# Kernel tuning notes

Hardware: AMD Instinct MI355X
Metric: run time of the kernel (lower is better)

## Reference

```python
import jax, jax.numpy as jnp
import numpy as np

E_PHI = 1024
E_F = 1024
HID = 1024
N_HEADS = 16
HEAD_DIM = HID // N_HEADS


def setup_inputs() -> dict:
    key = jax.random.key(0)
    ks = jax.random.split(key, 9)
    B, S = 2, 2048
    s = 0.02
    return {
        "q": jax.random.normal(ks[0], (B, S, E_PHI), jnp.float32),
        "k": jax.random.normal(ks[1], (B, S, E_PHI), jnp.float32),
        "v": jax.random.normal(ks[2], (B, S, E_F), jnp.float32),
        "W_q": jax.random.normal(ks[3], (E_PHI, HID), jnp.float32) * s,
        "W_k": jax.random.normal(ks[4], (E_PHI, HID), jnp.float32) * s,
        "W_v": jax.random.normal(ks[5], (E_F, HID), jnp.float32) * s,
        "b_v": jax.random.normal(ks[6], (HID,), jnp.float32) * s,
        "W_o": jax.random.normal(ks[7], (HID, E_F), jnp.float32) * s,
        "b_o": jax.random.normal(ks[8], (E_F,), jnp.float32) * s,
    }


def reference(q, k, v, W_q, W_k, W_v, b_v, W_o, b_o):
    B, S, _ = q.shape
    # projections -> [B, S, n_heads, head_dim]
    qh = (q @ W_q).reshape(B, S, N_HEADS, HEAD_DIM)
    kh = (k @ W_k).reshape(B, S, N_HEADS, HEAD_DIM)
    vh = (v @ W_v + b_v).reshape(B, S, N_HEADS, HEAD_DIM)

    scale = 1.0 / jnp.sqrt(jnp.float32(HEAD_DIM))
    # scores: [B, H, S_q, S_k]
    scores = jnp.einsum("bihd,bjhd->bhij", qh, kh) * scale

    i = jnp.arange(S)[:, None]
    j = jnp.arange(S)[None, :]
    # strict causal (j < i) plus the single (0,0) entry
    keep = (j < i) | ((i == 0) & (j == 0))
    scores = jnp.where(keep, scores, jnp.float32(-jnp.inf))

    probs = jax.nn.softmax(scores, axis=-1)
    attn = jnp.einsum("bhij,bjhd->bihd", probs, vh).reshape(B, S, HID)
    # dropout is identity in eval mode
    return attn @ W_o + b_o
```

## Files before the change

### kernel.cpp

```cpp
#include <hip/hip_runtime.h>
#include <hip/hip_bf16.h>

typedef __attribute__((ext_vector_type(8))) short bf16x8;
typedef __attribute__((ext_vector_type(4))) float f32x4;
typedef __attribute__((ext_vector_type(4))) unsigned u32x4;

typedef __attribute__((address_space(1))) const void gv_t;
typedef __attribute__((address_space(3))) void lv_t;

static __device__ __forceinline__ void gload16(const void* g, void* l) {
    __builtin_amdgcn_global_load_lds((gv_t*)g, (lv_t*)l, 16, 0, 0);
}

static __device__ __forceinline__ f32x4 mfma16(bf16x8 a, bf16x8 b, f32x4 c) {
    return __builtin_amdgcn_mfma_f32_16x16x32_bf16(a, b, c, 0, 0, 0);
}

static __device__ __forceinline__ unsigned short f2bf(float x) {
    __bf16 b = (__bf16)x;
    return __builtin_bit_cast(unsigned short, b);
}
static __device__ __forceinline__ unsigned pk2(float lo, float hi) {
    return (unsigned)f2bf(lo) | ((unsigned)f2bf(hi) << 16);
}

#define NN 1024
#define KK 1024
#define BK 32
#define NKT (KK / BK)
#define AP 72
#define SOFF2 17.3123404907f

__global__ void cvt3_k(const float* __restrict__ q, const float* __restrict__ k,
                       const float* __restrict__ v, unsigned short* __restrict__ dst)
{
    const int z = blockIdx.y;
    const float* src = (z == 0) ? q : (z == 1) ? k : v;
    unsigned short* d = dst + (size_t)z * 4194304u;
    const size_t i = ((size_t)blockIdx.x * 256 + threadIdx.x) * 8;
    float4 a = *reinterpret_cast<const float4*>(&src[i]);
    float4 b = *reinterpret_cast<const float4*>(&src[i + 4]);
    bf16x8 o;
    o[0] = (short)f2bf(a.x); o[1] = (short)f2bf(a.y);
    o[2] = (short)f2bf(a.z); o[3] = (short)f2bf(a.w);
    o[4] = (short)f2bf(b.x); o[5] = (short)f2bf(b.y);
    o[6] = (short)f2bf(b.z); o[7] = (short)f2bf(b.w);
    *reinterpret_cast<bf16x8*>(&d[i]) = o;
}

__global__ void trcvt_k(const float* __restrict__ w0, const float* __restrict__ w1,
                        const float* __restrict__ w2, const float* __restrict__ w3,
                        unsigned short* __restrict__ dst)
{
    const int z = blockIdx.z;
    const float* W = (z == 0) ? w0 : (z == 1) ? w1 : (z == 2) ? w2 : w3;
    unsigned short* D = dst + (size_t)z * 1048576u;
    __shared__ float t[32][33];
    const int tx = threadIdx.x, ty = threadIdx.y;
    const int x  = blockIdx.x * 32 + tx;
    const int y0 = blockIdx.y * 32;
    for (int i = ty; i < 32; i += 8) t[i][tx] = W[(size_t)(y0 + i) * 1024 + x];
    __syncthreads();
    const int xo = y0 + tx;
    for (int i = ty; i < 32; i += 8)
        D[(size_t)(blockIdx.x * 32 + i) * 1024 + xo] = f2bf(t[tx][i]);
}

template<int MODE, int TM, int MINB>
__global__ __launch_bounds__(256, MINB)
void gemm2_k(const unsigned short* __restrict__ Abase,
             const unsigned short* __restrict__ Btbase,
             void* __restrict__ Cbase,
             unsigned short* __restrict__ C2,
             const float* __restrict__ bias)
{
    constexpr int ACH = TM / 64;
    constexpr int NJ  = (TM == 128) ? 4 : 2;
    __shared__ unsigned short As[3][ACH * 2048];
    __shared__ unsigned short Bs[3][4096];

    const int f   = blockIdx.x;
    const int xcd = f & 7;
    const int g   = f >> 3;
    int z, bx, by;
    if (MODE == 0) {
        z  = g >> 5;
        const int rr = g & 31;
        bx = xcd * 4 + (rr & 3);
        by = rr >> 2;
    } else {
        z  = 0;
        bx = xcd * 8 + (g & 7);
        by = g >> 3;
    }

    const unsigned short* A  = Abase  + (size_t)z * 4194304u;
    const unsigned short* Bt = Btbase + (size_t)z * 1048576u;

    const int tid = threadIdx.x;
    const int wid = tid >> 6, lane = tid & 63;
    const int lg = lane >> 4, lc = lane & 15;
    const int brow = bx * TM;
    const int bcol = by * 128;
    const int wr = (TM == 128) ? (wid >> 1) * 64 : 0;
    const int wc = (TM == 128) ? (wid & 1) * 64  : wid * 32;

    const int srow = tid >> 2;
    const int scol = (tid & 3) * 8;

    f32x4 acc[4][NJ];
#pragma unroll
    for (int i = 0; i < 4; ++i)
#pragma unroll
        for (int j = 0; j < NJ; ++j) acc[i][j] = (f32x4){0.f, 0.f, 0.f, 0.f};

    auto issue_tile = [&](int kt, int c) {
        const int k0 = kt * BK;
#pragma unroll
        for (int ch = 0; ch < ACH; ++ch)
            gload16(&A[(size_t)(brow + ch * 64 + srow) * KK + k0 + scol], &As[c][ch * 2048 + tid * 8]);
        gload16(&Bt[(size_t)(bcol + srow)      * KK + k0 + scol], &Bs[c][tid * 8]);
        gload16(&Bt[(size_t)(bcol + 64 + srow) * KK + k0 + scol], &Bs[c][2048 + tid * 8]);
    };
    auto compute_tile = [&](int c) {
        bf16x8 af[4], bfr[NJ];
#pragma unroll
        for (int i = 0; i < 4; ++i)
            af[i] = *reinterpret_cast<const bf16x8*>(&As[c][(wr + i * 16 + lc) * 32 + lg * 8]);
#pragma unroll
        for (int j = 0; j < NJ; ++j)
            bfr[j] = *reinterpret_cast<const bf16x8*>(&Bs[c][(wc + j * 16 + lc) * 32 + lg * 8]);
#pragma unroll
        for (int i = 0; i < 4; ++i)
#pragma unroll
            for (int j = 0; j < NJ; ++j)
                acc[i][j] = mfma16(af[i], bfr[j], acc[i][j]);
    };

    issue_tile(0, 0);
    issue_tile(1, 1);

    int c0 = 0, c1 = 1, c2 = 2;
    for (int kt = 0; kt < NKT - 1; ++kt) {
        if (TM == 128) asm volatile("s_waitcnt vmcnt(4)" ::: "memory");
        else           asm volatile("s_waitcnt vmcnt(3)" ::: "memory");
        __builtin_amdgcn_s_barrier();
        __builtin_amdgcn_sched_barrier(0);
        if (kt + 2 < NKT) issue_tile(kt + 2, c2);
        compute_tile(c0);
        const int t = c0; c0 = c1; c1 = c2; c2 = t;
    }
    asm volatile("s_waitcnt vmcnt(0)" ::: "memory");
    __builtin_amdgcn_s_barrier();
    __builtin_amdgcn_sched_barrier(0);
    compute_tile(c0);

    float scale = 1.0f;
    const float* bp = nullptr;
    if (MODE == 0) { if (z == 0) scale = 0.18033688f; if (z == 2) bp = bias; }
    else           { bp = bias; }

    if (MODE == 0 && z == 2) {
#pragma unroll
        for (int j = 0; j < NJ; ++j) {
            const int col = bcol + wc + j * 16 + lc;
            const int h = col >> 6, d = col & 63;
            const float bb = bp[col];
#pragma unroll
            for (int i = 0; i < 4; ++i) {
                const int row0 = brow + wr + i * 16 + lg * 4;
                const int b = row0 >> 11, s0 = row0 & 2047;
                const size_t o = ((size_t)((b * 16 + h) * 64 + d)) * 2048u + s0;
                uint2 st;
                st.x = pk2(acc[i][j][0] + bb, acc[i][j][1] + bb);
                st.y = pk2(acc[i][j][2] + bb, acc[i][j][3] + bb);
                *reinterpret_cast<uint2*>(&C2[o]) = st;
            }
        }
    } else {
#pragma unroll
        for (int j = 0; j < NJ; ++j) {
            const int col = bcol + wc + j * 16 + lc;
            const float bb = bp ? bp[col] : 0.0f;
#pragma unroll
            for (int i = 0; i < 4; ++i) {
                const int row0 = brow + wr + i * 16 + lg * 4;
#pragma unroll
                for (int r = 0; r < 4; ++r) {
                    const float val = acc[i][j][r] * scale + bb;
                    if (MODE == 0)
                        ((unsigned short*)Cbase)[(size_t)z * 4194304u + (size_t)(row0 + r) * NN + col] = f2bf(val);
                    else
                        ((float*)Cbase)[(size_t)(row0 + r) * NN + col] = val;
                }
            }
        }
    }
}

__global__ __launch_bounds__(256, 4)
void attn_k(const unsigned short* __restrict__ qh,
            const unsigned short* __restrict__ kh,
            const unsigned short* __restrict__ vt,
            unsigned short* __restrict__ out)
{
    __shared__ unsigned short Ks[2][64 * AP];
    __shared__ unsigned short Vs[2][64 * AP];

    const int id = blockIdx.x;
    const int u  = id >> 5;
    const int qt = (u < 16) ? u : 47 - u;
    const int bh = (id & 7) * 4 + ((id >> 3) & 3);
    const int b = bh >> 4, h = bh & 15;
    const int tid = threadIdx.x, wid = tid >> 6, lane = tid & 63;
    const int lg = lane >> 4, lc = lane & 15;
    const int q0w = qt * 64 + wid * 16;

    const size_t base = (size_t)b * 2048u * 1024u + (size_t)h * 64u;
    const unsigned short* Qb  = qh + base;
    const unsigned short* Kb  = kh + base;
    const unsigned short* Vtb = vt + (size_t)bh * 131072u;

    const int r0 = tid >> 3, kof = (tid & 7) * 8;
    const int kperm = ((r0 & 12) << 1) | ((r0 >> 2) & 4) | (r0 & 3);

    bf16x8 qf[2];
#pragma unroll
    for (int s = 0; s < 2; ++s)
        qf[s] = *reinterpret_cast<const bf16x8*>(&Qb[(size_t)(q0w + lc) * 1024 + s * 32 + lg * 8]);

    f32x4 accT[4];
#pragma unroll
    for (int d = 0; d < 4; ++d) accT[d] = (f32x4){0.f, 0.f, 0.f, 0.f};
    float lsum = 0.f;

    bf16x8 ka0 = *reinterpret_cast<const bf16x8*>(&Kb [(size_t)(kperm)      * 1024 + kof]);
    bf16x8 ka1 = *reinterpret_cast<const bf16x8*>(&Kb [(size_t)(32 + kperm) * 1024 + kof]);
    bf16x8 va0 = *reinterpret_cast<const bf16x8*>(&Vtb[(size_t)(r0)      * 2048 + kof]);
    bf16x8 va1 = *reinterpret_cast<const bf16x8*>(&Vtb[(size_t)(32 + r0) * 2048 + kof]);

    for (int kt = 0; kt <= qt; ++kt) {
        const int cur = kt & 1;
        const int k0 = kt * 64;

        *reinterpret_cast<bf16x8*>(&Ks[cur][(r0)      * AP + kof]) = ka0;
        *reinterpret_cast<bf16x8*>(&Ks[cur][(32 + r0) * AP + kof]) = ka1;
        *reinterpret_cast<bf16x8*>(&Vs[cur][(r0)      * AP + kof]) = va0;
        *reinterpret_cast<bf16x8*>(&Vs[cur][(32 + r0) * AP + kof]) = va1;
        asm volatile("s_waitcnt lgkmcnt(0)" ::: "memory");
        __builtin_amdgcn_s_barrier();
        __builtin_amdgcn_sched_barrier(0);

        if (kt < qt) {
            const int kn = k0 + 64;
            ka0 = *reinterpret_cast<const bf16x8*>(&Kb [(size_t)(kn + kperm)      * 1024 + kof]);
            ka1 = *reinterpret_cast<const bf16x8*>(&Kb [(size_t)(kn + 32 + kperm) * 1024 + kof]);
            va0 = *reinterpret_cast<const bf16x8*>(&Vtb[(size_t)(r0)      * 2048 + kn + kof]);
            va1 = *reinterpret_cast<const bf16x8*>(&Vtb[(size_t)(32 + r0) * 2048 + kn + kof]);
        }

        f32x4 sc[4];
#pragma unroll
        for (int g = 0; g < 4; ++g) sc[g] = (f32x4){0.f, 0.f, 0.f, 0.f};
        __builtin_amdgcn_s_setprio(1);
#pragma unroll
        for (int s = 0; s < 2; ++s)
#pragma unroll
            for (int g = 0; g < 4; ++g) {
                bf16x8 kf = *reinterpret_cast<const bf16x8*>(
                    &Ks[cur][(g * 16 + lc) * AP + s * 32 + lg * 8]);
                sc[g] = mfma16(kf, qf[s], sc[g]);
            }
        __builtin_amdgcn_s_setprio(0);

        if (kt == qt) {
            const int qi = q0w + lc;
#pragma unroll
            for (int g = 0; g < 4; ++g)
#pragma unroll
                for (int r = 0; r < 4; ++r) {
                    const int ki = k0 + ((g & 2) << 4) + 8 * lg + 4 * (g & 1) + r;
                    const bool keep = (ki < qi) || (qi == 0 && ki == 0);
                    if (!keep) sc[g][r] = -1e30f;
                }
        }

        float p[4][4];
#pragma unroll
        for (int g = 0; g < 4; ++g)
#pragma unroll
            for (int r = 0; r < 4; ++r) {
                p[g][r] = exp2f(sc[g][r] - SOFF2);
                lsum += p[g][r];
            }

#pragma unroll
        for (int s = 0; s < 2; ++s) {
            u32x4 fr;
            fr[0] = pk2(p[2 * s][0],     p[2 * s][1]);
            fr[1] = pk2(p[2 * s][2],     p[2 * s][3]);
            fr[2] = pk2(p[2 * s + 1][0], p[2 * s + 1][1]);
            fr[3] = pk2(p[2 * s + 1][2], p[2 * s + 1][3]);
            bf16x8 pb = __builtin_bit_cast(bf16x8, fr);
            __builtin_amdgcn_s_setprio(1);
#pragma unroll
            for (int di = 0; di < 4; ++di) {
                bf16x8 vf = *reinterpret_cast<const bf16x8*>(
                    &Vs[cur][(di * 16 + lc) * AP + s * 32 + lg * 8]);
                accT[di] = mfma16(vf, pb, accT[di]);
            }
            __builtin_amdgcn_s_setprio(0);
        }
    }

    lsum += __shfl_xor(lsum, 16);
    lsum += __shfl_xor(lsum, 32);
    const float inv = 1.0f / lsum;

    const size_t orow = (size_t)(b * 2048 + q0w + lc) * 1024 + (size_t)h * 64 + lg * 4;
#pragma unroll
    for (int di = 0; di < 4; ++di) {
        unsigned lo  = pk2(accT[di][0] * inv, accT[di][1] * inv);
        unsigned hi2 = pk2(accT[di][2] * inv, accT[di][3] * inv);
        uint2 st; st.x = lo; st.y = hi2;
        *reinterpret_cast<uint2*>(&out[orow + di * 16]) = st;
    }
}

extern "C" void kernel_launch(void* const* d_in, const int* in_sizes, int n_in,
                              void* d_out, int out_size, void* d_ws, size_t ws_size,
                              hipStream_t stream)
{
    const float* q   = (const float*)d_in[0];
    const float* k   = (const float*)d_in[1];
    const float* v   = (const float*)d_in[2];
    const float* W_q = (const float*)d_in[3];
    const float* W_k = (const float*)d_in[4];
    const float* W_v = (const float*)d_in[5];
    const float* b_v = (const float*)d_in[6];
    const float* W_o = (const float*)d_in[7];
    const float* b_o = (const float*)d_in[8];

    char* w = (char*)d_ws;
    unsigned short* qkvb = (unsigned short*)w;
    unsigned short* Wt   = (unsigned short*)(w + 25165824);
    unsigned short* ph   = (unsigned short*)(w + 33554432);
    unsigned short* attn = (unsigned short*)(w + 58720256);
    unsigned short* vt   = ph + 2 * 4194304;

    cvt3_k <<<dim3(2048, 3, 1), 256, 0, stream>>>(q, k, v, qkvb);
    trcvt_k<<<dim3(32, 32, 4), dim3(32, 8, 1), 0, stream>>>(W_q, W_k, W_v, W_o, Wt);
    gemm2_k<0, 128, 3><<<dim3(768, 1, 1), 256, 0, stream>>>(qkvb, Wt, ph, vt, b_v);
    attn_k <<<dim3(1024, 1, 1), 256, 0, stream>>>(ph, ph + 4194304, vt, attn);
    gemm2_k<1, 64, 2><<<dim3(512, 1, 1), 256, 0, stream>>>(attn, Wt + 3 * 1048576, d_out, nullptr, b_o);
}
```

Before: 112.4 us.

## Double query tile per attention block to reuse K/V tiles across 128 rows

The attention kernel now gives each block 128 query rows instead of 64. Each wave handles two 16-row fragments, so each K/V tile loaded into shared memory feeds twice as many MFMAs. The grid is halved and the launch bounds drop to 2 waves per SIMD to make room for the doubled accumulators. The causal pairing of query blocks is kept, and fragments whose diagonal tile has already passed are skipped. The costs are lower occupancy, fewer blocks to hide latency, and some imbalance between the two fragments of a wave.

```diff
diff --git a/kernel.cpp b/kernel.cpp
--- a/kernel.cpp
+++ b/kernel.cpp
@@ -198,7 +198,7 @@
     }
 }
 
-__global__ __launch_bounds__(256, 4)
+__global__ __launch_bounds__(256, 2)
 void attn_k(const unsigned short* __restrict__ qh,
             const unsigned short* __restrict__ kh,
             const unsigned short* __restrict__ vt,
@@ -209,12 +209,15 @@
 
     const int id = blockIdx.x;
     const int u  = id >> 5;
-    const int qt = (u < 16) ? u : 47 - u;
+    const int qb = (u < 8) ? u : 23 - u;
     const int bh = (id & 7) * 4 + ((id >> 3) & 3);
     const int b = bh >> 4, h = bh & 15;
     const int tid = threadIdx.x, wid = tid >> 6, lane = tid & 63;
     const int lg = lane >> 4, lc = lane & 15;
-    const int q0w = qt * 64 + wid * 16;
+    const int q0 = qb * 128 + wid * 32;
+    const int dt0 = q0 >> 6;
+    const int dt1 = (q0 + 16) >> 6;
+    const int nkt = 2 * qb + 2;
 
     const size_t base = (size_t)b * 2048u * 1024u + (size_t)h * 64u;
     const unsigned short* Qb  = qh + base;
@@ -224,22 +227,27 @@
     const int r0 = tid >> 3, kof = (tid & 7) * 8;
     const int kperm = ((r0 & 12) << 1) | ((r0 >> 2) & 4) | (r0 & 3);
 
-    bf16x8 qf[2];
-#pragma unroll
-    for (int s = 0; s < 2; ++s)
-        qf[s] = *reinterpret_cast<const bf16x8*>(&Qb[(size_t)(q0w + lc) * 1024 + s * 32 + lg * 8]);
-
-    f32x4 accT[4];
-#pragma unroll
-    for (int d = 0; d < 4; ++d) accT[d] = (f32x4){0.f, 0.f, 0.f, 0.f};
-    float lsum = 0.f;
+    bf16x8 qf[2][2];
+#pragma unroll
+    for (int f = 0; f < 2; ++f)
+#pragma unroll
+        for (int s = 0; s < 2; ++s)
+            qf[f][s] = *reinterpret_cast<const bf16x8*>(
+                &Qb[(size_t)(q0 + f * 16 + lc) * 1024 + s * 32 + lg * 8]);
+
+    f32x4 accT[2][4];
+#pragma unroll
+    for (int f = 0; f < 2; ++f)
+#pragma unroll
+        for (int d = 0; d < 4; ++d) accT[f][d] = (f32x4){0.f, 0.f, 0.f, 0.f};
+    float lsum[2] = {0.f, 0.f};
 
     bf16x8 ka0 = *reinterpret_cast<const bf16x8*>(&Kb [(size_t)(kperm)      * 1024 + kof]);
     bf16x8 ka1 = *reinterpret_cast<const bf16x8*>(&Kb [(size_t)(32 + kperm) * 1024 + kof]);
     bf16x8 va0 = *reinterpret_cast<const bf16x8*>(&Vtb[(size_t)(r0)      * 2048 + kof]);
     bf16x8 va1 = *reinterpret_cast<const bf16x8*>(&Vtb[(size_t)(32 + r0) * 2048 + kof]);
 
-    for (int kt = 0; kt <= qt; ++kt) {
+    for (int kt = 0; kt < nkt; ++kt) {
         const int cur = kt & 1;
         const int k0 = kt * 64;
 
@@ -251,7 +259,7 @@
         __builtin_amdgcn_s_barrier();
         __builtin_amdgcn_sched_barrier(0);
 
-        if (kt < qt) {
+        if (kt + 1 < nkt) {
             const int kn = k0 + 64;
             ka0 = *reinterpret_cast<const bf16x8*>(&Kb [(size_t)(kn + kperm)      * 1024 + kof]);
             ka1 = *reinterpret_cast<const bf16x8*>(&Kb [(size_t)(kn + 32 + kperm) * 1024 + kof]);
@@ -259,9 +267,15 @@
             va1 = *reinterpret_cast<const bf16x8*>(&Vtb[(size_t)(32 + r0) * 2048 + kn + kof]);
         }
 
-        f32x4 sc[4];
-#pragma unroll
-        for (int g = 0; g < 4; ++g) sc[g] = (f32x4){0.f, 0.f, 0.f, 0.f};
+        const bool act0 = (kt <= dt0);
+        const bool act1 = (kt <= dt1);
+        if (!act1) continue;
+
+        f32x4 sc[2][4];
+#pragma unroll
+        for (int f = 0; f < 2; ++f)
+#pragma unroll
+            for (int g = 0; g < 4; ++g) sc[f][g] = (f32x4){0.f, 0.f, 0.f, 0.f};
         __builtin_amdgcn_s_setprio(1);
 #pragma unroll
         for (int s = 0; s < 2; ++s)
@@ -269,61 +283,78 @@
             for (int g = 0; g < 4; ++g) {
                 bf16x8 kf = *reinterpret_cast<const bf16x8*>(
                     &Ks[cur][(g * 16 + lc) * AP + s * 32 + lg * 8]);
-                sc[g] = mfma16(kf, qf[s], sc[g]);
+                sc[1][g] = mfma16(kf, qf[1][s], sc[1][g]);
+                if (act0) sc[0][g] = mfma16(kf, qf[0][s], sc[0][g]);
             }
         __builtin_amdgcn_s_setprio(0);
 
-        if (kt == qt) {
-            const int qi = q0w + lc;
+#pragma unroll
+        for (int f = 0; f < 2; ++f) {
+            if (kt == ((f == 0) ? dt0 : dt1)) {
+                const int qi = q0 + f * 16 + lc;
+#pragma unroll
+                for (int g = 0; g < 4; ++g)
+#pragma unroll
+                    for (int r = 0; r < 4; ++r) {
+                        const int ki = k0 + ((g & 2) << 4) + 8 * lg + 4 * (g & 1) + r;
+                        const bool keep = (ki < qi) || (qi == 0 && ki == 0);
+                        if (!keep) sc[f][g][r] = -1e30f;
+                    }
+            }
+        }
+
+        unsigned pw[2][2][4];
+#pragma unroll
+        for (int f = 0; f < 2; ++f) {
+            if (f == 0 && !act0) continue;
+            float p[4][4];
 #pragma unroll
             for (int g = 0; g < 4; ++g)
 #pragma unroll
                 for (int r = 0; r < 4; ++r) {
-                    const int ki = k0 + ((g & 2) << 4) + 8 * lg + 4 * (g & 1) + r;
-                    const bool keep = (ki < qi) || (qi == 0 && ki == 0);
-                    if (!keep) sc[g][r] = -1e30f;
+                    p[g][r] = exp2f(sc[f][g][r] - SOFF2);
+                    lsum[f] += p[g][r];
                 }
-        }
-
-        float p[4][4];
-#pragma unroll
-        for (int g = 0; g < 4; ++g)
-#pragma unroll
-            for (int r = 0; r < 4; ++r) {
-                p[g][r] = exp2f(sc[g][r] - SOFF2);
-                lsum += p[g][r];
-            }
+#pragma unroll
+            for (int s = 0; s < 2; ++s) {
+                pw[f][s][0] = pk2(p[2 * s][0],     p[2 * s][1]);
+                pw[f][s][1] = pk2(p[2 * s][2],     p[2 * s][3]);
+                pw[f][s][2] = pk2(p[2 * s + 1][0], p[2 * s + 1][1]);
+                pw[f][s][3] = pk2(p[2 * s + 1][2], p[2 * s + 1][3]);
+            }
+        }
 
 #pragma unroll
         for (int s = 0; s < 2; ++s) {
-            u32x4 fr;
-            fr[0] = pk2(p[2 * s][0],     p[2 * s][1]);
-            fr[1] = pk2(p[2 * s][2],     p[2 * s][3]);
-            fr[2] = pk2(p[2 * s + 1][0], p[2 * s + 1][1]);
-            fr[3] = pk2(p[2 * s + 1][2], p[2 * s + 1][3]);
-            bf16x8 pb = __builtin_bit_cast(bf16x8, fr);
+            bf16x8 pb1 = __builtin_bit_cast(bf16x8, *(const u32x4*)pw[1][s]);
+            bf16x8 pb0;
+            if (act0) pb0 = __builtin_bit_cast(bf16x8, *(const u32x4*)pw[0][s]);
             __builtin_amdgcn_s_setprio(1);
 #pragma unroll
             for (int di = 0; di < 4; ++di) {
                 bf16x8 vf = *reinterpret_cast<const bf16x8*>(
                     &Vs[cur][(di * 16 + lc) * AP + s * 32 + lg * 8]);
-                accT[di] = mfma16(vf, pb, accT[di]);
+                accT[1][di] = mfma16(vf, pb1, accT[1][di]);
+                if (act0) accT[0][di] = mfma16(vf, pb0, accT[0][di]);
             }
             __builtin_amdgcn_s_setprio(0);
         }
     }
 
-    lsum += __shfl_xor(lsum, 16);
-    lsum += __shfl_xor(lsum, 32);
-    const float inv = 1.0f / lsum;
-
-    const size_t orow = (size_t)(b * 2048 + q0w + lc) * 1024 + (size_t)h * 64 + lg * 4;
-#pragma unroll
-    for (int di = 0; di < 4; ++di) {
-        unsigned lo  = pk2(accT[di][0] * inv, accT[di][1] * inv);
-        unsigned hi2 = pk2(accT[di][2] * inv, accT[di][3] * inv);
-        uint2 st; st.x = lo; st.y = hi2;
-        *reinterpret_cast<uint2*>(&out[orow + di * 16]) = st;
+#pragma unroll
+    for (int f = 0; f < 2; ++f) {
+        float ls = lsum[f];
+        ls += __shfl_xor(ls, 16);
+        ls += __shfl_xor(ls, 32);
+        const float inv = 1.0f / ls;
+        const size_t orow = (size_t)(b * 2048 + q0 + f * 16 + lc) * 1024 + (size_t)h * 64 + lg * 4;
+#pragma unroll
+        for (int di = 0; di < 4; ++di) {
+            unsigned lo  = pk2(accT[f][di][0] * inv, accT[f][di][1] * inv);
+            unsigned hi2 = pk2(accT[f][di][2] * inv, accT[f][di][3] * inv);
+            uint2 st; st.x = lo; st.y = hi2;
+            *reinterpret_cast<uint2*>(&out[orow + di * 16]) = st;
+        }
     }
 }
 
@@ -351,6 +382,6 @@
     cvt3_k <<<dim3(2048, 3, 1), 256, 0, stream>>>(q, k, v, qkvb);
     trcvt_k<<<dim3(32, 32, 4), dim3(32, 8, 1), 0, stream>>>(W_q, W_k, W_v, W_o, Wt);
     gemm2_k<0, 128, 3><<<dim3(768, 1, 1), 256, 0, stream>>>(qkvb, Wt, ph, vt, b_v);
-    attn_k <<<dim3(1024, 1, 1), 256, 0, stream>>>(ph, ph + 4194304, vt, attn);
+    attn_k <<<dim3(512, 1, 1), 256, 0, stream>>>(ph, ph + 4194304, vt, attn);
     gemm2_k<1, 64, 2><<<dim3(512, 1, 1), 256, 0, stream>>>(attn, Wt + 3 * 1048576, d_out, nullptr, b_o);
 }
```

Measured after the change: 120.0 us. 1.07x slower.
